# Kernel tuning notes

Hardware: AMD Instinct MI355X
Metric: run time of the kernel (lower is better)

Reference implementation:

```python
import jax, jax.numpy as jnp
import numpy as np

B, D, K = 65536, 512, 64
H1, H2 = 256, 128
START_TEMP, MIN_TEMP, NR_EPOCHS = 10.0, 0.1, 1000


def setup_inputs() -> dict:
    key = jax.random.key(0)
    ks = jax.random.split(key, 12)
    x = jax.random.normal(ks[0], (B, D), dtype=jnp.float32)
    label = jax.random.normal(ks[1], (B, 1), dtype=jnp.float32)
    u = jax.random.uniform(ks[2], (B, K), dtype=jnp.float32, minval=1e-6, maxval=1.0)
    # MLP params: D -> H1 -> H2 -> K (relu on hidden layers, bias everywhere)
    W1 = jax.random.normal(ks[3], (D, H1), dtype=jnp.float32) / np.sqrt(D)
    b1 = jnp.zeros((H1,), dtype=jnp.float32)
    W2 = jax.random.normal(ks[4], (H1, H2), dtype=jnp.float32) / np.sqrt(H1)
    b2 = jnp.zeros((H2,), dtype=jnp.float32)
    W3 = jax.random.normal(ks[5], (H2, K), dtype=jnp.float32) / np.sqrt(H2)
    b3 = jnp.zeros((K,), dtype=jnp.float32)
    # thetas ~ Uniform(0,1) per torch init.uniform_
    thetas = jax.random.uniform(ks[6], (D, K), dtype=jnp.float32)
    return {"x": x, "label": label, "u": u, "W1": W1, "b1": b1,
            "W2": W2, "b2": b2, "W3": W3, "b3": b3,
            "thetas": thetas, "epoch": 100}


def _current_temp(epoch):
    # exponential schedule: max(min_temp, start*(min/start)**(epoch/nr_epochs))
    t = START_TEMP * (MIN_TEMP / START_TEMP) ** (epoch / NR_EPOCHS)
    return jnp.maximum(jnp.float32(MIN_TEMP), jnp.float32(t))


def reference(x, label, u, W1, b1, W2, b2, W3, b3, thetas, epoch):
    # MLP -> logits [B, K]
    h = jax.nn.relu(x @ W1 + b1)
    h = jax.nn.relu(h @ W2 + b2)
    logits = h @ W3 + b3
    # Concrete (Gumbel-softmax) feature selection over the K candidate predictors
    xt = x @ thetas                      # [B, K]
    gumbel = -jnp.log(-jnp.log(u))
    temp = _current_temp(jnp.float32(epoch))
    weights = jax.nn.softmax((logits + gumbel) / temp, axis=1)
    # diagonal(xt @ weights.T) == row-wise dot product (O(B*K), not O(B^2*K))
    selected = jnp.sum(xt * weights, axis=1, keepdims=True)  # [B, 1]
    loss = jnp.mean((selected - label) ** 2)
    return loss
```

## Files before the change

kernel.cpp:

```cpp
#include <hip/hip_runtime.h>
#include <math.h>

#define Bn  65536
#define Dn  512
#define Kn  64
#define H1n 256
#define H2n 128
#define BM  32

typedef short bf16x8 __attribute__((ext_vector_type(8)));
typedef float floatx4 __attribute__((ext_vector_type(4)));

__device__ __forceinline__ unsigned short f2bf(float f) {
    unsigned u = __builtin_bit_cast(unsigned, f);
    u += 0x7FFF + ((u >> 16) & 1);
    return (unsigned short)(u >> 16);
}

__global__ __launch_bounds__(256)
void prep_k(const float* __restrict__ W1, const float* __restrict__ W2,
            const float* __restrict__ W3, const float* __restrict__ Th,
            unsigned short* __restrict__ ws)
{
    const int gid = blockIdx.x * 256 + threadIdx.x;
    if (gid < 131072) {
        const int s = gid, k = s >> 8, n = s & 255;
        const int dst = (((n >> 4) * 16 + (k >> 5)) * 64 + ((k >> 3) & 3) * 16 + (n & 15)) * 8 + (k & 7);
        ws[dst] = f2bf(W1[s]);
    } else if (gid < 163840) {
        const int s = gid - 131072, k = s >> 6, n = s & 63;
        const int dst = 131072 + (((n >> 4) * 16 + (k >> 5)) * 64 + ((k >> 3) & 3) * 16 + (n & 15)) * 8 + (k & 7);
        ws[dst] = f2bf(Th[s]);
    } else if (gid < 196608) {
        const int s = gid - 163840, k = s >> 7, n = s & 127;
        const int dst = 163840 + (((n >> 4) * 8 + (k >> 5)) * 64 + ((k >> 3) & 3) * 16 + (n & 15)) * 8 + (k & 7);
        ws[dst] = f2bf(W2[s]);
    } else if (gid < 204800) {
        const int s = gid - 196608, k = s >> 6, n = s & 63;
        const int dst = 196608 + (((n >> 4) * 4 + (k >> 5)) * 64 + ((k >> 3) & 3) * 16 + (n & 15)) * 8 + (k & 7);
        ws[dst] = f2bf(W3[s]);
    }
}

__global__ __launch_bounds__(1024)
void reduce_k(const float* __restrict__ p, float* __restrict__ out)
{
    __shared__ float sred[16];
    const int tid = threadIdx.x;
    float s = 0.f;
    #pragma unroll
    for (int i = 0; i < 8; ++i) s += p[tid + i * 1024];
    #pragma unroll
    for (int off = 32; off > 0; off >>= 1) s += __shfl_xor(s, off);
    if ((tid & 63) == 0) sred[tid >> 6] = s;
    __syncthreads();
    if (tid < 64) {
        float v = (tid < 16) ? sred[tid] : 0.f;
        #pragma unroll
        for (int off = 8; off > 0; off >>= 1) v += __shfl_xor(v, off);
        if (tid == 0) out[0] = v * (1.0f / (float)Bn);
    }
}

__global__ __launch_bounds__(256, 4)
void llp_mfma(const float* __restrict__ x,
              const float* __restrict__ label,
              const float* __restrict__ u,
              const float* __restrict__ b1, const float* __restrict__ b2,
              const float* __restrict__ b3,
              const unsigned short* __restrict__ W1f,
              const unsigned short* __restrict__ Tf,
              const unsigned short* __restrict__ W2f,
              const unsigned short* __restrict__ W3f,
              const int* __restrict__ epoch_p,
              float* __restrict__ partials)
{
    __shared__ char smem[32768];

    const int tid  = threadIdx.x;
    const int row0 = blockIdx.x * BM;
    const int w    = tid >> 6;
    const int lane = tid & 63;
    const int lrow = lane & 15;
    const int quad = lane >> 4;

    float upf[8], labpf[8];
    #pragma unroll
    for (int rr = 0; rr < 8; ++rr) {
        upf[rr]   = u[(size_t)(row0 + w * 8 + rr) * Kn + lane];
        labpf[rr] = label[row0 + w * 8 + rr];
    }

    {
        const float4* xg4 = (const float4*)(x + (size_t)row0 * Dn);
        #pragma unroll
        for (int i = 0; i < 16; ++i) {
            const int f = tid + i * 256;
            const float4 v = xg4[f];
            const int row = f >> 7, c4 = f & 127;
            const int kb = c4 >> 1, half = c4 & 1;
            ushort4 o;
            o.x = f2bf(v.x); o.y = f2bf(v.y); o.z = f2bf(v.z); o.w = f2bf(v.w);
            *(ushort4*)(smem + ((row * 64 + (kb ^ (row & 7))) << 4) + (half << 3)) = o;
        }
    }
    __syncthreads();

    const int ct0 = w * 4;
    floatx4 acc[2][5];
    #pragma unroll
    for (int t = 0; t < 4; ++t) {
        const float bv = b1[(ct0 + t) * 16 + lrow];
        acc[0][t] = (floatx4){bv, bv, bv, bv};
        acc[1][t] = (floatx4){bv, bv, bv, bv};
    }
    acc[0][4] = (floatx4){0.f, 0.f, 0.f, 0.f};
    acc[1][4] = (floatx4){0.f, 0.f, 0.f, 0.f};

    bf16x8 aB[2][2], bB[2][5];
    #pragma unroll
    for (int rt = 0; rt < 2; ++rt)
        aB[0][rt] = *(const bf16x8*)(smem +
                        (((rt * 16 + lrow) * 64 + (quad ^ (lrow & 7))) << 4));
    #pragma unroll
    for (int t = 0; t < 4; ++t)
        bB[0][t] = *(const bf16x8*)(W1f + ((((ct0 + t) * 16 + 0) * 64 + lane) << 3));
    bB[0][4] = *(const bf16x8*)(Tf + (((w * 16 + 0) * 64 + lane) << 3));

    #pragma unroll
    for (int ks = 0; ks < 16; ++ks) {
        const int cur = ks & 1, nxt = cur ^ 1;
        if (ks < 15) {
            const int kn = ks + 1;
            #pragma unroll
            for (int rt = 0; rt < 2; ++rt)
                aB[nxt][rt] = *(const bf16x8*)(smem +
                    (((rt * 16 + lrow) * 64 + ((kn * 4 + quad) ^ (lrow & 7))) << 4));
            #pragma unroll
            for (int t = 0; t < 4; ++t)
                bB[nxt][t] = *(const bf16x8*)(W1f + ((((ct0 + t) * 16 + kn) * 64 + lane) << 3));
            bB[nxt][4] = *(const bf16x8*)(Tf + (((w * 16 + kn) * 64 + lane) << 3));
        }
        #pragma unroll
        for (int t = 0; t < 5; ++t) {
            acc[0][t] = __builtin_amdgcn_mfma_f32_16x16x32_bf16(aB[cur][0], bB[cur][t], acc[0][t], 0, 0, 0);
            acc[1][t] = __builtin_amdgcn_mfma_f32_16x16x32_bf16(aB[cur][1], bB[cur][t], acc[1][t], 0, 0, 0);
        }
    }
    __syncthreads();

    #pragma unroll
    for (int rt = 0; rt < 2; ++rt) {
        #pragma unroll
        for (int t = 0; t < 4; ++t) {
            const int col = (ct0 + t) * 16 + lrow;
            #pragma unroll
            for (int g = 0; g < 4; ++g) {
                const int orow = rt * 16 + quad * 4 + g;
                *(unsigned short*)(smem +
                    ((orow * 32 + ((col >> 3) ^ (orow & 7))) << 4) + ((col & 7) << 1))
                    = f2bf(fmaxf(acc[rt][t][g], 0.0f));
            }
        }
    }
    {
        float* xtf = (float*)(smem + 16384);
        #pragma unroll
        for (int rt = 0; rt < 2; ++rt)
            #pragma unroll
            for (int g = 0; g < 4; ++g)
                xtf[(rt * 16 + quad * 4 + g) * 64 + w * 16 + lrow] = acc[rt][4][g];
    }
    __syncthreads();

    const int c20 = w * 2;
    floatx4 acc2[2][2];
    #pragma unroll
    for (int i = 0; i < 2; ++i) {
        const float bv = b2[(c20 + i) * 16 + lrow];
        acc2[0][i] = (floatx4){bv, bv, bv, bv};
        acc2[1][i] = (floatx4){bv, bv, bv, bv};
    }
    bf16x8 a2[2][2], b2B[2][2];
    #pragma unroll
    for (int rt = 0; rt < 2; ++rt)
        a2[0][rt] = *(const bf16x8*)(smem +
                        (((rt * 16 + lrow) * 32 + (quad ^ (lrow & 7))) << 4));
    #pragma unroll
    for (int i = 0; i < 2; ++i)
        b2B[0][i] = *(const bf16x8*)(W2f + ((((c20 + i) * 8 + 0) * 64 + lane) << 3));

    #pragma unroll
    for (int ks = 0; ks < 8; ++ks) {
        const int cur = ks & 1, nxt = cur ^ 1;
        if (ks < 7) {
            const int kn = ks + 1;
            #pragma unroll
            for (int rt = 0; rt < 2; ++rt)
                a2[nxt][rt] = *(const bf16x8*)(smem +
                    (((rt * 16 + lrow) * 32 + ((kn * 4 + quad) ^ (lrow & 7))) << 4));
            #pragma unroll
            for (int i = 0; i < 2; ++i)
                b2B[nxt][i] = *(const bf16x8*)(W2f + ((((c20 + i) * 8 + kn) * 64 + lane) << 3));
        }
        #pragma unroll
        for (int i = 0; i < 2; ++i) {
            acc2[0][i] = __builtin_amdgcn_mfma_f32_16x16x32_bf16(a2[cur][0], b2B[cur][i], acc2[0][i], 0, 0, 0);
            acc2[1][i] = __builtin_amdgcn_mfma_f32_16x16x32_bf16(a2[cur][1], b2B[cur][i], acc2[1][i], 0, 0, 0);
        }
    }
    #pragma unroll
    for (int rt = 0; rt < 2; ++rt) {
        #pragma unroll
        for (int i = 0; i < 2; ++i) {
            const int col = (c20 + i) * 16 + lrow;
            #pragma unroll
            for (int g = 0; g < 4; ++g) {
                const int orow = rt * 16 + quad * 4 + g;
                *(unsigned short*)(smem + 24576 +
                    ((orow * 16 + ((col >> 3) ^ (orow & 7))) << 4) + ((col & 7) << 1))
                    = f2bf(fmaxf(acc2[rt][i][g], 0.0f));
            }
        }
    }
    __syncthreads();

    floatx4 acc3[2];
    {
        const float bv = b3[w * 16 + lrow];
        acc3[0] = (floatx4){bv, bv, bv, bv};
        acc3[1] = (floatx4){bv, bv, bv, bv};
    }
    #pragma unroll
    for (int ks = 0; ks < 4; ++ks) {
        const bf16x8 bb = *(const bf16x8*)(W3f + (((w * 4 + ks) * 64 + lane) << 3));
        #pragma unroll
        for (int rt = 0; rt < 2; ++rt) {
            const bf16x8 aa = *(const bf16x8*)(smem + 24576 +
                (((rt * 16 + lrow) * 16 + ((ks * 4 + quad) ^ (lrow & 7))) << 4));
            acc3[rt] = __builtin_amdgcn_mfma_f32_16x16x32_bf16(aa, bb, acc3[rt], 0, 0, 0);
        }
    }
    {
        float* lgf = (float*)smem;
        #pragma unroll
        for (int rt = 0; rt < 2; ++rt)
            #pragma unroll
            for (int g = 0; g < 4; ++g)
                lgf[(rt * 16 + quad * 4 + g) * 64 + w * 16 + lrow] = acc3[rt][g];
    }
    __syncthreads();

    {
        const float* lgf = (const float*)smem;
        const float* xtf = (const float*)(smem + 16384);
        const int ep = *epoch_p;
        const float tmp = 10.0f * powf(0.01f, (float)ep * 0.001f);
        const float inv_temp = 1.0f / fmaxf(0.1f, tmp);

        float partial = 0.0f;
        #pragma unroll
        for (int rr = 0; rr < 8; ++rr) {
            const int rw = w * 8 + rr;
            const float g = -logf(-logf(upf[rr]));
            float s = (lgf[rw * 64 + lane] + g) * inv_temp;
            float m = s;
            #pragma unroll
            for (int off = 32; off > 0; off >>= 1)
                m = fmaxf(m, __shfl_xor(m, off));
            const float e = expf(s - m);
            float sum = e;
            #pragma unroll
            for (int off = 32; off > 0; off >>= 1)
                sum += __shfl_xor(sum, off);
            float v = (e / sum) * xtf[rw * 64 + lane];
            #pragma unroll
            for (int off = 32; off > 0; off >>= 1)
                v += __shfl_xor(v, off);
            const float diff = v - labpf[rr];
            partial = fmaf(diff, diff, partial);
        }
        if (lane == 0)
            partials[blockIdx.x * 4 + w] = partial;
    }
}

extern "C" void kernel_launch(void* const* d_in, const int* in_sizes, int n_in,
                              void* d_out, int out_size, void* d_ws, size_t ws_size,
                              hipStream_t stream) {
    const float* x      = (const float*)d_in[0];
    const float* label  = (const float*)d_in[1];
    const float* u      = (const float*)d_in[2];
    const float* W1     = (const float*)d_in[3];
    const float* b1     = (const float*)d_in[4];
    const float* W2     = (const float*)d_in[5];
    const float* b2     = (const float*)d_in[6];
    const float* W3     = (const float*)d_in[7];
    const float* b3     = (const float*)d_in[8];
    const float* thetas = (const float*)d_in[9];
    const int*   epoch  = (const int*)d_in[10];
    float* out = (float*)d_out;

    unsigned short* wsb = (unsigned short*)d_ws;
    float* partials = (float*)((char*)d_ws + 409600);

    prep_k<<<800, 256, 0, stream>>>(W1, W2, W3, thetas, wsb);
    llp_mfma<<<Bn / BM, 256, 0, stream>>>(x, label, u, b1, b2, b3,
                                          wsb, wsb + 131072, wsb + 163840, wsb + 196608,
                                          epoch, partials);
    reduce_k<<<1, 1024, 0, stream>>>(partials, out);
}
```

Before: 261.9 us.

## Deepen MFMA operand prefetch, hoist weight loads before barriers, swizzle fp32 LDS tiles

Moves weight-fragment global loads ahead of the barriers so they overlap the x staging and the previous stage's LDS writes. The layer-1 and layer-2 loops now prefetch two k-steps ahead instead of one. The u and label loads are deferred until after layer 1, which lowers register pressure early in the kernel. Also switches the f32 to bf16 conversion to the packed v_cvt_pk_bf16_f32 instruction and XOR-swizzles the fp32 logits and xt LDS stores to cut bank conflicts. This gains latency hiding at the cost of more live registers, which may lower occupancy. The packed conversion may also round slightly differently from the manual routine.

```diff
diff --git a/kernel.cpp b/kernel.cpp
--- a/kernel.cpp
+++ b/kernel.cpp
@@ -15,6 +15,12 @@
     unsigned u = __builtin_bit_cast(unsigned, f);
     u += 0x7FFF + ((u >> 16) & 1);
     return (unsigned short)(u >> 16);
+}
+
+__device__ __forceinline__ unsigned cvt_pk_bf16(float lo, float hi) {
+    unsigned r;
+    asm("v_cvt_pk_bf16_f32 %0, %1, %2" : "=v"(r) : "v"(lo), "v"(hi));
+    return r;
 }
 
 __global__ __launch_bounds__(256)
@@ -84,13 +90,6 @@
     const int lrow = lane & 15;
     const int quad = lane >> 4;
 
-    float upf[8], labpf[8];
-    #pragma unroll
-    for (int rr = 0; rr < 8; ++rr) {
-        upf[rr]   = u[(size_t)(row0 + w * 8 + rr) * Kn + lane];
-        labpf[rr] = label[row0 + w * 8 + rr];
-    }
-
     {
         const float4* xg4 = (const float4*)(x + (size_t)row0 * Dn);
         #pragma unroll
@@ -99,14 +98,24 @@
             const float4 v = xg4[f];
             const int row = f >> 7, c4 = f & 127;
             const int kb = c4 >> 1, half = c4 & 1;
-            ushort4 o;
-            o.x = f2bf(v.x); o.y = f2bf(v.y); o.z = f2bf(v.z); o.w = f2bf(v.w);
-            *(ushort4*)(smem + ((row * 64 + (kb ^ (row & 7))) << 4) + (half << 3)) = o;
-        }
-    }
-    __syncthreads();
+            uint2 o2;
+            o2.x = cvt_pk_bf16(v.x, v.y);
+            o2.y = cvt_pk_bf16(v.z, v.w);
+            *(uint2*)(smem + ((row * 64 + (kb ^ (row & 7))) << 4) + (half << 3)) = o2;
+        }
+    }
 
     const int ct0 = w * 4;
+    bf16x8 aB[2][2], bB[2][5];
+    #pragma unroll
+    for (int p = 0; p < 2; ++p) {
+        #pragma unroll
+        for (int t = 0; t < 4; ++t)
+            bB[p][t] = *(const bf16x8*)(W1f + ((((ct0 + t) * 16 + p) * 64 + lane) << 3));
+        bB[p][4] = *(const bf16x8*)(Tf + (((w * 16 + p) * 64 + lane) << 3));
+    }
+    __syncthreads();
+
     floatx4 acc[2][5];
     #pragma unroll
     for (int t = 0; t < 4; ++t) {
@@ -117,34 +126,31 @@
     acc[0][4] = (floatx4){0.f, 0.f, 0.f, 0.f};
     acc[1][4] = (floatx4){0.f, 0.f, 0.f, 0.f};
 
-    bf16x8 aB[2][2], bB[2][5];
-    #pragma unroll
-    for (int rt = 0; rt < 2; ++rt)
-        aB[0][rt] = *(const bf16x8*)(smem +
-                        (((rt * 16 + lrow) * 64 + (quad ^ (lrow & 7))) << 4));
-    #pragma unroll
-    for (int t = 0; t < 4; ++t)
-        bB[0][t] = *(const bf16x8*)(W1f + ((((ct0 + t) * 16 + 0) * 64 + lane) << 3));
-    bB[0][4] = *(const bf16x8*)(Tf + (((w * 16 + 0) * 64 + lane) << 3));
+    #pragma unroll
+    for (int p = 0; p < 2; ++p)
+        #pragma unroll
+        for (int rt = 0; rt < 2; ++rt)
+            aB[p][rt] = *(const bf16x8*)(smem +
+                (((rt * 16 + lrow) * 64 + ((p * 4 + quad) ^ (lrow & 7))) << 4));
 
     #pragma unroll
     for (int ks = 0; ks < 16; ++ks) {
-        const int cur = ks & 1, nxt = cur ^ 1;
-        if (ks < 15) {
-            const int kn = ks + 1;
-            #pragma unroll
-            for (int rt = 0; rt < 2; ++rt)
-                aB[nxt][rt] = *(const bf16x8*)(smem +
-                    (((rt * 16 + lrow) * 64 + ((kn * 4 + quad) ^ (lrow & 7))) << 4));
-            #pragma unroll
-            for (int t = 0; t < 4; ++t)
-                bB[nxt][t] = *(const bf16x8*)(W1f + ((((ct0 + t) * 16 + kn) * 64 + lane) << 3));
-            bB[nxt][4] = *(const bf16x8*)(Tf + (((w * 16 + kn) * 64 + lane) << 3));
-        }
+        const int cur = ks & 1;
         #pragma unroll
         for (int t = 0; t < 5; ++t) {
             acc[0][t] = __builtin_amdgcn_mfma_f32_16x16x32_bf16(aB[cur][0], bB[cur][t], acc[0][t], 0, 0, 0);
             acc[1][t] = __builtin_amdgcn_mfma_f32_16x16x32_bf16(aB[cur][1], bB[cur][t], acc[1][t], 0, 0, 0);
+        }
+        if (ks < 14) {
+            const int kn = ks + 2;
+            #pragma unroll
+            for (int rt = 0; rt < 2; ++rt)
+                aB[cur][rt] = *(const bf16x8*)(smem +
+                    (((rt * 16 + lrow) * 64 + ((kn * 4 + quad) ^ (lrow & 7))) << 4));
+            #pragma unroll
+            for (int t = 0; t < 4; ++t)
+                bB[cur][t] = *(const bf16x8*)(W1f + ((((ct0 + t) * 16 + kn) * 64 + lane) << 3));
+            bB[cur][4] = *(const bf16x8*)(Tf + (((w * 16 + kn) * 64 + lane) << 3));
         }
     }
     __syncthreads();
@@ -165,15 +171,29 @@
     }
     {
         float* xtf = (float*)(smem + 16384);
+        const int xcol = (w * 16 + lrow) ^ (quad << 4);
         #pragma unroll
         for (int rt = 0; rt < 2; ++rt)
             #pragma unroll
             for (int g = 0; g < 4; ++g)
-                xtf[(rt * 16 + quad * 4 + g) * 64 + w * 16 + lrow] = acc[rt][4][g];
-    }
-    __syncthreads();
+                xtf[(rt * 16 + quad * 4 + g) * 64 + xcol] = acc[rt][4][g];
+    }
 
     const int c20 = w * 2;
+    bf16x8 a2[2][2], b2B[2][2];
+    #pragma unroll
+    for (int p = 0; p < 2; ++p)
+        #pragma unroll
+        for (int i = 0; i < 2; ++i)
+            b2B[p][i] = *(const bf16x8*)(W2f + ((((c20 + i) * 8 + p) * 64 + lane) << 3));
+    float upf[8], labpf[8];
+    #pragma unroll
+    for (int rr = 0; rr < 8; ++rr) {
+        upf[rr]   = u[(size_t)(row0 + w * 8 + rr) * Kn + lane];
+        labpf[rr] = label[row0 + w * 8 + rr];
+    }
+    __syncthreads();
+
     floatx4 acc2[2][2];
     #pragma unroll
     for (int i = 0; i < 2; ++i) {
@@ -181,32 +201,30 @@
         acc2[0][i] = (floatx4){bv, bv, bv, bv};
         acc2[1][i] = (floatx4){bv, bv, bv, bv};
     }
-    bf16x8 a2[2][2], b2B[2][2];
-    #pragma unroll
-    for (int rt = 0; rt < 2; ++rt)
-        a2[0][rt] = *(const bf16x8*)(smem +
-                        (((rt * 16 + lrow) * 32 + (quad ^ (lrow & 7))) << 4));
-    #pragma unroll
-    for (int i = 0; i < 2; ++i)
-        b2B[0][i] = *(const bf16x8*)(W2f + ((((c20 + i) * 8 + 0) * 64 + lane) << 3));
+    #pragma unroll
+    for (int p = 0; p < 2; ++p)
+        #pragma unroll
+        for (int rt = 0; rt < 2; ++rt)
+            a2[p][rt] = *(const bf16x8*)(smem +
+                (((rt * 16 + lrow) * 32 + ((p * 4 + quad) ^ (lrow & 7))) << 4));
 
     #pragma unroll
     for (int ks = 0; ks < 8; ++ks) {
-        const int cur = ks & 1, nxt = cur ^ 1;
-        if (ks < 7) {
-            const int kn = ks + 1;
-            #pragma unroll
-            for (int rt = 0; rt < 2; ++rt)
-                a2[nxt][rt] = *(const bf16x8*)(smem +
-                    (((rt * 16 + lrow) * 32 + ((kn * 4 + quad) ^ (lrow & 7))) << 4));
-            #pragma unroll
-            for (int i = 0; i < 2; ++i)
-                b2B[nxt][i] = *(const bf16x8*)(W2f + ((((c20 + i) * 8 + kn) * 64 + lane) << 3));
-        }
+        const int cur = ks & 1;
         #pragma unroll
         for (int i = 0; i < 2; ++i) {
             acc2[0][i] = __builtin_amdgcn_mfma_f32_16x16x32_bf16(a2[cur][0], b2B[cur][i], acc2[0][i], 0, 0, 0);
             acc2[1][i] = __builtin_amdgcn_mfma_f32_16x16x32_bf16(a2[cur][1], b2B[cur][i], acc2[1][i], 0, 0, 0);
+        }
+        if (ks < 6) {
+            const int kn = ks + 2;
+            #pragma unroll
+            for (int rt = 0; rt < 2; ++rt)
+                a2[cur][rt] = *(const bf16x8*)(smem +
+                    (((rt * 16 + lrow) * 32 + ((kn * 4 + quad) ^ (lrow & 7))) << 4));
+            #pragma unroll
+            for (int i = 0; i < 2; ++i)
+                b2B[cur][i] = *(const bf16x8*)(W2f + ((((c20 + i) * 8 + kn) * 64 + lane) << 3));
         }
     }
     #pragma unroll
@@ -223,6 +241,11 @@
             }
         }
     }
+
+    bf16x8 bb[4];
+    #pragma unroll
+    for (int ks = 0; ks < 4; ++ks)
+        bb[ks] = *(const bf16x8*)(W3f + (((w * 4 + ks) * 64 + lane) << 3));
     __syncthreads();
 
     floatx4 acc3[2];
@@ -231,23 +254,28 @@
         acc3[0] = (floatx4){bv, bv, bv, bv};
         acc3[1] = (floatx4){bv, bv, bv, bv};
     }
-    #pragma unroll
-    for (int ks = 0; ks < 4; ++ks) {
-        const bf16x8 bb = *(const bf16x8*)(W3f + (((w * 4 + ks) * 64 + lane) << 3));
-        #pragma unroll
-        for (int rt = 0; rt < 2; ++rt) {
-            const bf16x8 aa = *(const bf16x8*)(smem + 24576 +
-                (((rt * 16 + lrow) * 16 + ((ks * 4 + quad) ^ (lrow & 7))) << 4));
-            acc3[rt] = __builtin_amdgcn_mfma_f32_16x16x32_bf16(aa, bb, acc3[rt], 0, 0, 0);
-        }
+    {
+        bf16x8 aa[2][4];
+        #pragma unroll
+        for (int ks = 0; ks < 4; ++ks)
+            #pragma unroll
+            for (int rt = 0; rt < 2; ++rt)
+                aa[rt][ks] = *(const bf16x8*)(smem + 24576 +
+                    (((rt * 16 + lrow) * 16 + ((ks * 4 + quad) ^ (lrow & 7))) << 4));
+        #pragma unroll
+        for (int ks = 0; ks < 4; ++ks)
+            #pragma unroll
+            for (int rt = 0; rt < 2; ++rt)
+                acc3[rt] = __builtin_amdgcn_mfma_f32_16x16x32_bf16(aa[rt][ks], bb[ks], acc3[rt], 0, 0, 0);
     }
     {
         float* lgf = (float*)smem;
+        const int xcol = (w * 16 + lrow) ^ (quad << 4);
         #pragma unroll
         for (int rt = 0; rt < 2; ++rt)
             #pragma unroll
             for (int g = 0; g < 4; ++g)
-                lgf[(rt * 16 + quad * 4 + g) * 64 + w * 16 + lrow] = acc3[rt][g];
+                lgf[(rt * 16 + quad * 4 + g) * 64 + xcol] = acc3[rt][g];
     }
     __syncthreads();
 
@@ -262,8 +290,9 @@
         #pragma unroll
         for (int rr = 0; rr < 8; ++rr) {
             const int rw = w * 8 + rr;
+            const int rlane = lane ^ ((rw & 12) << 2);
             const float g = -logf(-logf(upf[rr]));
-            float s = (lgf[rw * 64 + lane] + g) * inv_temp;
+            float s = (lgf[rw * 64 + rlane] + g) * inv_temp;
             float m = s;
             #pragma unroll
             for (int off = 32; off > 0; off >>= 1)
@@ -273,7 +302,7 @@
             #pragma unroll
             for (int off = 32; off > 0; off >>= 1)
                 sum += __shfl_xor(sum, off);
-            float v = (e / sum) * xtf[rw * 64 + lane];
+            float v = (e / sum) * xtf[rw * 64 + rlane];
             #pragma unroll
             for (int off = 32; off > 0; off >>= 1)
                 v += __shfl_xor(v, off);
```

After: 261.9 us. No clear change (-0.0%).
